# Optimization experiments

Measured on AMD Instinct MI355X. Metric: run time of the kernel, lower is better.

Reference implementation:

```python
import jax, jax.numpy as jnp
import numpy as np
from jax import lax

B, N, IN, OUT, RANK, P = 8, 7057, 1024, 1024, 64, 84
ALPHA = 1
SCALING = ALPHA / RANK
RATES = (2, 1, 4)


def _cubic(t):
    # PyTorch bicubic kernel (a = -0.75)
    a = -0.75
    at = jnp.abs(t)
    w1 = ((a + 2.0) * at - (a + 3.0)) * at * at + 1.0
    w2 = (((at - 5.0) * at + 8.0) * at - 4.0) * a
    return jnp.where(at <= 1.0, w1, jnp.where(at < 2.0, w2, 0.0))


def _resize_axis(x, out_size, axis):
    # 1-D bicubic resize along `axis`, align_corners=False, border replicate
    in_size = x.shape[axis]
    scale = in_size / out_size
    src = (jnp.arange(out_size, dtype=jnp.float32) + 0.5) * scale - 0.5
    i0 = jnp.floor(src)
    offs = jnp.arange(-1, 3, dtype=jnp.float32)[:, None]  # [4,1]
    pos = i0[None, :] + offs                              # [4,out]
    w = _cubic(src[None, :] - pos)                        # [4,out]
    idx = jnp.clip(pos.astype(jnp.int32), 0, in_size - 1)
    g = jnp.take(x, idx, axis=axis)  # axis -> (4, out)
    wshape = [1] * g.ndim
    wshape[axis] = 4
    wshape[axis + 1] = out_size
    return jnp.sum(g * w.reshape(wshape), axis=axis)


def _bicubic(x, h, w):
    # x: [B,C,H,W] -> [B,C,h,w]
    x = _resize_axis(x, h, axis=2)
    return _resize_axis(x, w, axis=3)


def _expert(x, cw, cb, rate):
    # x: [B,C,H,W]; cw: [C,C,3,3]; cb: [C]
    b, c, h, w = x.shape
    y = _bicubic(x, h * rate, w * rate)
    y = lax.conv_general_dilated(y, cw, (1, 1), [(1, 1), (1, 1)],
                                 dimension_numbers=('NCHW', 'OIHW', 'NCHW'))
    y = y + cb[None, :, None, None]
    y = _bicubic(y, h, w)
    return y.transpose(0, 2, 3, 1).reshape(b, h * w, c)  # [B,HW,C]


def setup_inputs() -> dict:
    key = jax.random.key(0)
    ks = jax.random.split(key, 9)
    return {
        'x': jax.random.normal(ks[0], (B, N, IN), dtype=jnp.float32),
        'W0': jax.random.normal(ks[1], (OUT, IN), dtype=jnp.float32) * 0.02,
        'b0': jax.random.normal(ks[2], (OUT,), dtype=jnp.float32) * 0.02,
        'W_down': jax.random.normal(ks[3], (RANK, IN), dtype=jnp.float32) * 0.02,
        'W_gate': jax.random.uniform(ks[4], (3, RANK), dtype=jnp.float32),
        'b_gate': jax.random.normal(ks[5], (3,), dtype=jnp.float32) * 0.02,
        'conv_w': jax.random.normal(ks[6], (3, RANK, RANK, 3, 3), dtype=jnp.float32) * 0.05,
        'conv_b': jax.random.normal(ks[7], (3, RANK), dtype=jnp.float32) * 0.02,
        'W_up': jax.random.normal(ks[8], (OUT, RANK), dtype=jnp.float32) * 0.02,
    }


def reference(x, W0, b0, W_down, W_gate, b_gate, conv_w, conv_b, W_up):
    out = jnp.einsum('bni,oi->bno', x, W0) + b0            # original layer
    z = jnp.einsum('bni,ri->bnr', x, W_down)               # lora_down (dropout p=0)
    cls_embed = z[:, :1]                                    # [B,1,R]
    feat = z[:, 1:].reshape(B, P, P, RANK).transpose(0, 3, 1, 2)  # [B,R,P,P]
    pooled = feat.mean(axis=(2, 3))                         # AdaptiveAvgPool2d(1)
    gate_score = pooled @ W_gate.T + b_gate                 # [B,3]
    gate_idx = jnp.argmax(gate_score, axis=-1)              # [B]
    eouts = jnp.stack([_expert(feat, conv_w[i], conv_b[i], RATES[i])
                       for i in range(3)], axis=0)          # [3,B,HW,R]
    sel = eouts[gate_idx, jnp.arange(B)] * SCALING          # [B,HW,R]
    lora = jnp.concatenate([cls_embed, sel], axis=1)        # [B,N,R]
    lora_out = jnp.einsum('bnr,or->bno', lora, W_up)
    return out + lora_out
```

## Files before the change

kernel.cpp:

```cpp
#include <hip/hip_runtime.h>
#include <stdint.h>

typedef unsigned short u16;
typedef __bf16 bf16x8 __attribute__((ext_vector_type(8)));
typedef float f32x4 __attribute__((ext_vector_type(4)));

#define B_ 8
#define N_ 7057
#define MTOT 56456
#define SCALING_F (1.0f/64.0f)

#define Z_OFF    0ull
#define LORA_OFF 14452736ull
#define GIDX_OFF 21679104ull
#define CWT_OFF  21679360ull
#define W0B_OFF  21900544ull
#define WDB_OFF  23997696ull
#define WUB_OFF  24128768ull
#define UP_OFF   24259840ull
#define CO_OFF   139865344ull
#define UPB_STRIDE ((size_t)112896 * 64)

__device__ __forceinline__ u16 f2b(float f) {
  __bf16 h = (__bf16)f;
  union { __bf16 h; u16 u; } v; v.h = h; return v.u;
}
__device__ __forceinline__ float b2f(u16 u) {
  union { uint32_t i; float f; } v; v.i = ((uint32_t)u) << 16; return v.f;
}
__device__ __forceinline__ void gload_lds16(const void* g, void* l) {
  __builtin_amdgcn_global_load_lds(
      (const __attribute__((address_space(1))) uint32_t*)g,
      (__attribute__((address_space(3))) uint32_t*)l, 16, 0, 0);
}
__device__ __forceinline__ f32x4 mfma16(bf16x8 a, bf16x8 b, f32x4 c) {
  return __builtin_amdgcn_mfma_f32_16x16x32_bf16(a, b, c, 0, 0, 0);
}
__device__ __forceinline__ void cvt_store8(u16* dst, float4 a, float4 b) {
  bf16x8 v;
  v[0] = (__bf16)a.x; v[1] = (__bf16)a.y; v[2] = (__bf16)a.z; v[3] = (__bf16)a.w;
  v[4] = (__bf16)b.x; v[5] = (__bf16)b.y; v[6] = (__bf16)b.z; v[7] = (__bf16)b.w;
  *(bf16x8*)dst = v;
}
__device__ __forceinline__ float cubicw(float t) {
  const float a = -0.75f;
  float at = fabsf(t);
  float w1 = ((a + 2.0f) * at - (a + 3.0f)) * at * at + 1.0f;
  float w2 = (((at - 5.0f) * at + 8.0f) * at - 4.0f) * a;
  return at <= 1.0f ? w1 : (at < 2.0f ? w2 : 0.0f);
}
__device__ __forceinline__ int iclamp(int v, int lo, int hi) { return v < lo ? lo : (v > hi ? hi : v); }
__device__ __forceinline__ int rate_of(int e) { return e == 0 ? 2 : (e == 1 ? 1 : 4); }

__global__ __launch_bounds__(256) void cvtall_kernel(const float* __restrict__ W0, const float* __restrict__ Wd,
                                                     const float* __restrict__ Wup, u16* __restrict__ dst) {
  int i = (blockIdx.x * 256 + threadIdx.x) * 4;
  if (i >= 1179648) return;
  const float* src;
  if (i < 1048576)      src = W0 + i;
  else if (i < 1114112) src = Wd + (i - 1048576);
  else                  src = Wup + (i - 1114112);
  float4 v = *(const float4*)src;
  union { u16 u[4]; uint2 q; } p;
  p.u[0] = f2b(v.x); p.u[1] = f2b(v.y); p.u[2] = f2b(v.z); p.u[3] = f2b(v.w);
  *(uint2*)(dst + i) = p.q;
}

__global__ __launch_bounds__(256) void zgemm_kernel(const float* __restrict__ x,
                                                    const u16* __restrict__ Wdb,
                                                    float* __restrict__ z) {
  __shared__ u16 As[64 * 32];
  __shared__ u16 Bs[64 * 32];
  const int tid = threadIdx.x;
  const int lane = tid & 63;
  const int w = tid >> 6;
  const int row0 = blockIdx.x * 64;
  f32x4 acc[4] = {{0,0,0,0},{0,0,0,0},{0,0,0,0},{0,0,0,0}};
  const int srow = tid >> 2, sk8 = tid & 3;
  int arow = row0 + srow; if (arow >= MTOT) arow = MTOT - 1;
  const float* agf = x + (size_t)arow * 1024 + sk8 * 8;
  const u16* bg = Wdb + (size_t)srow * 1024 + sk8 * 8;
  u16* al = As + tid * 8;
  u16* bl = Bs + tid * 8;
  const int klo = (lane >> 4) * 8;
  for (int k0 = 0; k0 < 1024; k0 += 32) {
    gload_lds16(bg + k0, bl);
    float4 q0 = *(const float4*)(agf + k0);
    float4 q1 = *(const float4*)(agf + k0 + 4);
    cvt_store8(al, q0, q1);
    __syncthreads();
    bf16x8 a = *(const bf16x8*)(As + (w * 16 + (lane & 15)) * 32 + klo);
#pragma unroll
    for (int fc = 0; fc < 4; ++fc) {
      bf16x8 bb = *(const bf16x8*)(Bs + (fc * 16 + (lane & 15)) * 32 + klo);
      acc[fc] = mfma16(a, bb, acc[fc]);
    }
    __syncthreads();
  }
  const int crow = (lane >> 4) * 4, ccol = lane & 15;
#pragma unroll
  for (int fc = 0; fc < 4; ++fc) {
#pragma unroll
    for (int i = 0; i < 4; ++i) {
      int gr = row0 + w * 16 + crow + i;
      if (gr < MTOT) z[(size_t)gr * 64 + fc * 16 + ccol] = acc[fc][i];
    }
  }
}

__global__ __launch_bounds__(256) void convwt_kernel(const float* __restrict__ cw, u16* __restrict__ cwt) {
  int idx = blockIdx.x * 256 + threadIdx.x;
  if (idx >= 3 * 9 * 64 * 64) return;
  int ci = idx & 63;
  int co = (idx >> 6) & 63;
  int rest = idx >> 12;
  int tap = rest % 9;
  int e = rest / 9;
  cwt[idx] = f2b(cw[((size_t)(e * 64 + co) * 64 + ci) * 9 + tap]);
}

__global__ __launch_bounds__(256) void gate1_kernel(const float* __restrict__ z, float* __restrict__ pp) {
  int b = blockIdx.y, q = blockIdx.x;
  int tid = threadIdx.x;
  int c = tid & 63, part = tid >> 6;
  const float* zb = z + (size_t)b * N_ * 64;
  int n0 = 1 + q * 126;
  float s = 0.0f;
  for (int n = n0 + part; n < n0 + 126; n += 4) s += zb[(size_t)n * 64 + c];
  __shared__ float red[4][64];
  red[part][c] = s;
  __syncthreads();
  if (tid < 64)
    pp[((size_t)b * 56 + q) * 64 + tid] = red[0][tid] + red[1][tid] + red[2][tid] + red[3][tid];
}

__global__ __launch_bounds__(64) void gate2_kernel(const float* __restrict__ pp, const float* __restrict__ z,
                                                   const float* __restrict__ Wg, const float* __restrict__ bg,
                                                   int* __restrict__ gidx, u16* __restrict__ lora) {
  int b = blockIdx.x;
  int c = threadIdx.x;
  float s = 0.0f;
  for (int q = 0; q < 56; ++q) s += pp[((size_t)b * 56 + q) * 64 + c];
  __shared__ float pl[64];
  pl[c] = s * (1.0f / 7056.0f);
  const float* zb = z + (size_t)b * N_ * 64;
  lora[(size_t)b * N_ * 64 + c] = f2b(zb[c]);
  __syncthreads();
  if (c == 0) {
    float best = 0.0f; int bi = 0;
    for (int e = 0; e < 3; ++e) {
      float sc = bg[e];
      for (int r = 0; r < 64; ++r) sc += pl[r] * Wg[e * 64 + r];
      if (e == 0 || sc > best) { best = sc; bi = e; }
    }
    gidx[b] = bi;
  }
}

__global__ __launch_bounds__(256) void up_kernel(const float* __restrict__ z, const int* __restrict__ gidx,
                                                 u16* __restrict__ up) {
  int b = blockIdx.z;
  int r = rate_of(gidx[b]);
  int H = 84 * r;
  int y = blockIdx.y; if (y >= H) return;
  int c = threadIdx.x & 63, s = threadIdx.x >> 6;
  int x0 = blockIdx.x * 16 + s * 4;
  if (x0 >= H) return;
  float inv = 1.0f / (float)r;
  float sy = (y + 0.5f) * inv - 0.5f;
  float fy = floorf(sy);
  int iy0 = (int)fy;
  float wy[4]; int yi[4];
#pragma unroll
  for (int u = 0; u < 4; ++u) { wy[u] = cubicw(sy - (fy - 1.0f + u)); yi[u] = iclamp(iy0 - 1 + u, 0, 83); }
  const float* zb = z + ((size_t)b * N_ + 1) * 64;
  u16* ub = up + (size_t)b * UPB_STRIDE;
#pragma unroll
  for (int xx = 0; xx < 4; ++xx) {
    int X = x0 + xx; if (X >= H) break;
    float sx = (X + 0.5f) * inv - 0.5f;
    float fx = floorf(sx);
    int ix0 = (int)fx;
    float acc = 0.0f;
#pragma unroll
    for (int v = 0; v < 4; ++v) {
      float wv = cubicw(sx - (fx - 1.0f + v));
      int xiv = iclamp(ix0 - 1 + v, 0, 83);
#pragma unroll
      for (int u = 0; u < 4; ++u)
        acc += wy[u] * wv * zb[((size_t)yi[u] * 84 + xiv) * 64 + c];
    }
    ub[((size_t)y * H + X) * 64 + c] = f2b(acc);
  }
}

__global__ __launch_bounds__(256) void conv_kernel(const u16* __restrict__ up, const u16* __restrict__ cwt,
                                                   const float* __restrict__ cb, const int* __restrict__ gidx,
                                                   u16* __restrict__ cvo) {
  int b = blockIdx.z;
  int e = gidx[b];
  int r = rate_of(e);
  int H = 84 * r;
  int tx = blockIdx.x, ty = blockIdx.y;
  if (tx * 8 >= H || ty * 8 >= H) return;
  __shared__ u16 halo[100 * 64];
  __shared__ u16 Bw[2][4096];
  int tid = threadIdx.x, lane = tid & 63, w = tid >> 6;
  const u16* ub = up + (size_t)b * UPB_STRIDE;
  const u16* wte = cwt + (size_t)e * 9 * 4096;
  gload_lds16(wte + tid * 8, Bw[0] + tid * 8);
  gload_lds16(wte + 2048 + tid * 8, Bw[0] + 2048 + tid * 8);
  for (int li = tid; li < 800; li += 256) {
    int pix = li >> 3, cq = li & 7;
    int hy = pix / 10, hx = pix - hy * 10;
    int iy = ty * 8 - 1 + hy, ix = tx * 8 - 1 + hx;
    uint4 v = {0u, 0u, 0u, 0u};
    if (iy >= 0 && iy < H && ix >= 0 && ix < H)
      v = *(const uint4*)(ub + ((size_t)iy * H + ix) * 64 + cq * 8);
    *(uint4*)(halo + pix * 64 + cq * 8) = v;
  }
  __syncthreads();
  f32x4 acc[4] = {{0,0,0,0},{0,0,0,0},{0,0,0,0},{0,0,0,0}};
  int p = w * 16 + (lane & 15);
  int py = p >> 3, px = p & 7;
  int klo = (lane >> 4) * 8;
  for (int tap = 0; tap < 9; ++tap) {
    if (tap < 8) {
      const u16* wt = wte + (size_t)(tap + 1) * 4096;
      gload_lds16(wt + tid * 8, Bw[(tap + 1) & 1] + tid * 8);
      gload_lds16(wt + 2048 + tid * 8, Bw[(tap + 1) & 1] + 2048 + tid * 8);
    }
    int dy = tap / 3, dx = tap - dy * 3;
    const u16* hb = halo + ((py + dy) * 10 + (px + dx)) * 64 + klo;
    const u16* bwc = Bw[tap & 1];
#pragma unroll
    for (int kk = 0; kk < 2; ++kk) {
      bf16x8 a = *(const bf16x8*)(hb + kk * 32);
#pragma unroll
      for (int fc = 0; fc < 4; ++fc) {
        bf16x8 bb = *(const bf16x8*)(bwc + (fc * 16 + (lane & 15)) * 64 + kk * 32 + klo);
        acc[fc] = mfma16(a, bb, acc[fc]);
      }
    }
    __syncthreads();
  }
  int crow = (lane >> 4) * 4, ccol = lane & 15;
  u16* cvb = cvo + (size_t)b * UPB_STRIDE;
#pragma unroll
  for (int fc = 0; fc < 4; ++fc) {
    int co = fc * 16 + ccol;
    float bias = cb[e * 64 + co];
#pragma unroll
    for (int i = 0; i < 4; ++i) {
      int pd = w * 16 + crow + i;
      int gy = ty * 8 + (pd >> 3), gx = tx * 8 + (pd & 7);
      if (gy < H && gx < H)
        cvb[((size_t)gy * H + gx) * 64 + co] = f2b(acc[fc][i] + bias);
    }
  }
}

__global__ __launch_bounds__(256) void down_kernel(const u16* __restrict__ cvo, const int* __restrict__ gidx,
                                                   u16* __restrict__ lora) {
  int b = blockIdx.z;
  int r = rate_of(gidx[b]);
  int H = 84 * r;
  int tid = threadIdx.x;
  int c = tid & 63, s = tid >> 6;
  int y = blockIdx.y;
  int x = blockIdx.x * 4 + s;
  float fr = (float)r;
  float sy = (y + 0.5f) * fr - 0.5f;
  float fy = floorf(sy);
  int iy0 = (int)fy;
  float wy[4]; int yi[4];
#pragma unroll
  for (int u = 0; u < 4; ++u) { wy[u] = cubicw(sy - (fy - 1.0f + u)); yi[u] = iclamp(iy0 - 1 + u, 0, H - 1); }
  float sx = (x + 0.5f) * fr - 0.5f;
  float fx = floorf(sx);
  int ix0 = (int)fx;
  float wx[4]; int xi[4];
#pragma unroll
  for (int v = 0; v < 4; ++v) { wx[v] = cubicw(sx - (fx - 1.0f + v)); xi[v] = iclamp(ix0 - 1 + v, 0, H - 1); }
  const u16* cbase = cvo + (size_t)b * UPB_STRIDE;
  float acc = 0.0f;
#pragma unroll
  for (int u = 0; u < 4; ++u)
#pragma unroll
    for (int v = 0; v < 4; ++v)
      acc += wy[u] * wx[v] * b2f(cbase[((size_t)yi[u] * H + xi[v]) * 64 + c]);
  lora[((size_t)b * N_ + 1 + y * 84 + x) * 64 + c] = f2b(acc * SCALING_F);
}

#define MAIN_COMPUTE()                                                                       \
  {                                                                                          \
    bf16x8 af[4], bfr[4];                                                                    \
    _Pragma("unroll")                                                                        \
    for (int fm = 0; fm < 4; ++fm)                                                           \
      af[fm] = *(const bf16x8*)(As + (wr * 64 + fm * 16 + (lane & 15)) * 32 + klo);          \
    _Pragma("unroll")                                                                        \
    for (int fc = 0; fc < 4; ++fc)                                                           \
      bfr[fc] = *(const bf16x8*)(Bs + (wc * 64 + fc * 16 + (lane & 15)) * 32 + klo);         \
    _Pragma("unroll")                                                                        \
    for (int fm = 0; fm < 4; ++fm) {                                                         \
      _Pragma("unroll")                                                                      \
      for (int fc = 0; fc < 4; ++fc)                                                         \
        acc[fm][fc] = mfma16(af[fm], bfr[fc], acc[fm][fc]);                                  \
    }                                                                                        \
  }

__global__ __launch_bounds__(256) void main_gemm(const float* __restrict__ x, const u16* __restrict__ W0b,
                                                 const float* __restrict__ b0, const u16* __restrict__ lora,
                                                 const u16* __restrict__ Wub, float* __restrict__ out) {
  __shared__ u16 As[128 * 32];
  __shared__ u16 Bs[128 * 32];
  int tid = threadIdx.x, lane = tid & 63, w = tid >> 6;
  int bid = blockIdx.x;
  int wg = (bid & 7) * 442 + (bid >> 3);
  int row0 = (wg >> 3) * 128, col0 = (wg & 7) * 128;
  int wr = w >> 1, wc = w & 1;
  f32x4 acc[4][4] = {};
  int srow = tid >> 2, sk8 = tid & 3;
  int ar0 = row0 + srow; if (ar0 >= MTOT) ar0 = MTOT - 1;
  int ar1 = row0 + srow + 64; if (ar1 >= MTOT) ar1 = MTOT - 1;
  const float* agf0 = x + (size_t)ar0 * 1024 + sk8 * 8;
  const float* agf1 = x + (size_t)ar1 * 1024 + sk8 * 8;
  const u16* bg0 = W0b + (size_t)(col0 + srow) * 1024 + sk8 * 8;
  const u16* bg1 = W0b + (size_t)(col0 + srow + 64) * 1024 + sk8 * 8;
  u16* al0 = As + tid * 8; u16* al1 = As + tid * 8 + 2048;
  u16* bl0 = Bs + tid * 8; u16* bl1 = Bs + tid * 8 + 2048;
  const int klo = (lane >> 4) * 8;
  for (int k0 = 0; k0 < 1024; k0 += 32) {
    gload_lds16(bg0 + k0, bl0);
    gload_lds16(bg1 + k0, bl1);
    float4 q0 = *(const float4*)(agf0 + k0);
    float4 q1 = *(const float4*)(agf0 + k0 + 4);
    float4 q2 = *(const float4*)(agf1 + k0);
    float4 q3 = *(const float4*)(agf1 + k0 + 4);
    cvt_store8(al0, q0, q1);
    cvt_store8(al1, q2, q3);
    __syncthreads();
    MAIN_COMPUTE();
    __syncthreads();
  }
  const u16* lg0 = lora + (size_t)ar0 * 64 + sk8 * 8;
  const u16* lg1 = lora + (size_t)ar1 * 64 + sk8 * 8;
  const u16* ug0 = Wub + (size_t)(col0 + srow) * 64 + sk8 * 8;
  const u16* ug1 = Wub + (size_t)(col0 + srow + 64) * 64 + sk8 * 8;
  for (int k0 = 0; k0 < 64; k0 += 32) {
    gload_lds16(lg0 + k0, al0);
    gload_lds16(lg1 + k0, al1);
    gload_lds16(ug0 + k0, bl0);
    gload_lds16(ug1 + k0, bl1);
    __syncthreads();
    MAIN_COMPUTE();
    __syncthreads();
  }
  int crow = (lane >> 4) * 4, ccol = lane & 15;
#pragma unroll
  for (int fm = 0; fm < 4; ++fm) {
    int grb = row0 + wr * 64 + fm * 16 + crow;
#pragma unroll
    for (int fc = 0; fc < 4; ++fc) {
      int gc = col0 + wc * 64 + fc * 16 + ccol;
      float bias = b0[gc];
#pragma unroll
      for (int i = 0; i < 4; ++i) {
        int gr = grb + i;
        if (gr < MTOT) out[(size_t)gr * 1024 + gc] = acc[fm][fc][i] + bias;
      }
    }
  }
}

extern "C" void kernel_launch(void* const* d_in, const int* in_sizes, int n_in,
                              void* d_out, int out_size, void* d_ws, size_t ws_size,
                              hipStream_t stream) {
  const float* x   = (const float*)d_in[0];
  const float* W0  = (const float*)d_in[1];
  const float* b0  = (const float*)d_in[2];
  const float* Wd  = (const float*)d_in[3];
  const float* Wg  = (const float*)d_in[4];
  const float* bg  = (const float*)d_in[5];
  const float* cw  = (const float*)d_in[6];
  const float* cb  = (const float*)d_in[7];
  const float* Wup = (const float*)d_in[8];
  char* ws = (char*)d_ws;
  float* z    = (float*)(ws + Z_OFF);
  u16* lora   = (u16*)(ws + LORA_OFF);
  int* gidx   = (int*)(ws + GIDX_OFF);
  u16* cwt    = (u16*)(ws + CWT_OFF);
  u16* W0b    = (u16*)(ws + W0B_OFF);
  u16* Wub    = (u16*)(ws + WUB_OFF);
  u16* up     = (u16*)(ws + UP_OFF);
  float* pp   = (float*)(ws + UP_OFF);
  u16* cvo    = (u16*)(ws + CO_OFF);
  float* out  = (float*)d_out;
  u16* Wdb    = (u16*)(ws + WDB_OFF);

  cvtall_kernel<<<dim3(1152), dim3(256), 0, stream>>>(W0, Wd, Wup, W0b);
  convwt_kernel<<<dim3(432), dim3(256), 0, stream>>>(cw, cwt);
  zgemm_kernel<<<dim3(883), dim3(256), 0, stream>>>(x, Wdb, z);
  gate1_kernel<<<dim3(56, 8), dim3(256), 0, stream>>>(z, pp);
  gate2_kernel<<<dim3(8), dim3(64), 0, stream>>>(pp, z, Wg, bg, gidx, lora);
  up_kernel<<<dim3(21, 336, 8), dim3(256), 0, stream>>>(z, gidx, up);
  conv_kernel<<<dim3(42, 42, 8), dim3(256), 0, stream>>>(up, cwt, cb, gidx, cvo);
  down_kernel<<<dim3(21, 84, 8), dim3(256), 0, stream>>>(cvo, gidx, lora);
  main_gemm<<<dim3(3536), dim3(256), 0, stream>>>(x, W0b, b0, lora, Wub, out);
}
```

Before: 642.9 us.

## Pre-convert x to bf16 in zgemm and stream it to main GEMM via LDS DMA

Measured after the change: 595.7 us. 1.08x faster.

```diff
diff --git a/kernel.cpp b/kernel.cpp
--- a/kernel.cpp
+++ b/kernel.cpp
@@ -19,6 +19,9 @@
 #define WUB_OFF  24128768ull
 #define UP_OFF   24259840ull
 #define CO_OFF   139865344ull
+#define XB_OFF   255470848ull
+#define WS_FAST  371092736ull
+#define WS_SLOW  255487232ull
 #define UPB_STRIDE ((size_t)112896 * 64)
 
 __device__ __forceinline__ u16 f2b(float f) {
@@ -36,11 +39,11 @@
 __device__ __forceinline__ f32x4 mfma16(bf16x8 a, bf16x8 b, f32x4 c) {
   return __builtin_amdgcn_mfma_f32_16x16x32_bf16(a, b, c, 0, 0, 0);
 }
-__device__ __forceinline__ void cvt_store8(u16* dst, float4 a, float4 b) {
+__device__ __forceinline__ bf16x8 cvt8(float4 a, float4 b) {
   bf16x8 v;
   v[0] = (__bf16)a.x; v[1] = (__bf16)a.y; v[2] = (__bf16)a.z; v[3] = (__bf16)a.w;
   v[4] = (__bf16)b.x; v[5] = (__bf16)b.y; v[6] = (__bf16)b.z; v[7] = (__bf16)b.w;
-  *(bf16x8*)dst = v;
+  return v;
 }
 __device__ __forceinline__ float cubicw(float t) {
   const float a = -0.75f;
@@ -66,9 +69,19 @@
   *(uint2*)(dst + i) = p.q;
 }
 
+__global__ __launch_bounds__(256) void cvtx_kernel(const float* __restrict__ x, u16* __restrict__ xb) {
+  size_t stride = (size_t)gridDim.x * 256 * 8;
+  for (size_t i = ((size_t)blockIdx.x * 256 + threadIdx.x) * 8; i < (size_t)MTOT * 1024; i += stride) {
+    float4 a = *(const float4*)(x + i);
+    float4 b = *(const float4*)(x + i + 4);
+    *(bf16x8*)(xb + i) = cvt8(a, b);
+  }
+}
+
 __global__ __launch_bounds__(256) void zgemm_kernel(const float* __restrict__ x,
                                                     const u16* __restrict__ Wdb,
-                                                    float* __restrict__ z) {
+                                                    float* __restrict__ z,
+                                                    u16* __restrict__ xb) {
   __shared__ u16 As[64 * 32];
   __shared__ u16 Bs[64 * 32];
   const int tid = threadIdx.x;
@@ -80,6 +93,7 @@
   int arow = row0 + srow; if (arow >= MTOT) arow = MTOT - 1;
   const float* agf = x + (size_t)arow * 1024 + sk8 * 8;
   const u16* bg = Wdb + (size_t)srow * 1024 + sk8 * 8;
+  u16* xbp = xb ? (xb + (size_t)arow * 1024 + sk8 * 8) : nullptr;
   u16* al = As + tid * 8;
   u16* bl = Bs + tid * 8;
   const int klo = (lane >> 4) * 8;
@@ -87,7 +101,9 @@
     gload_lds16(bg + k0, bl);
     float4 q0 = *(const float4*)(agf + k0);
     float4 q1 = *(const float4*)(agf + k0 + 4);
-    cvt_store8(al, q0, q1);
+    bf16x8 cv = cvt8(q0, q1);
+    *(bf16x8*)al = cv;
+    if (xbp) *(bf16x8*)(xbp + k0) = cv;
     __syncthreads();
     bf16x8 a = *(const bf16x8*)(As + (w * 16 + (lane & 15)) * 32 + klo);
 #pragma unroll
@@ -292,70 +308,80 @@
   lora[((size_t)b * N_ + 1 + y * 84 + x) * 64 + c] = f2b(acc * SCALING_F);
 }
 
-#define MAIN_COMPUTE()                                                                       \
-  {                                                                                          \
-    bf16x8 af[4], bfr[4];                                                                    \
-    _Pragma("unroll")                                                                        \
-    for (int fm = 0; fm < 4; ++fm)                                                           \
-      af[fm] = *(const bf16x8*)(As + (wr * 64 + fm * 16 + (lane & 15)) * 32 + klo);          \
-    _Pragma("unroll")                                                                        \
-    for (int fc = 0; fc < 4; ++fc)                                                           \
-      bfr[fc] = *(const bf16x8*)(Bs + (wc * 64 + fc * 16 + (lane & 15)) * 32 + klo);         \
-    _Pragma("unroll")                                                                        \
-    for (int fm = 0; fm < 4; ++fm) {                                                         \
-      _Pragma("unroll")                                                                      \
-      for (int fc = 0; fc < 4; ++fc)                                                         \
-        acc[fm][fc] = mfma16(af[fm], bfr[fc], acc[fm][fc]);                                  \
-    }                                                                                        \
-  }
-
-__global__ __launch_bounds__(256) void main_gemm(const float* __restrict__ x, const u16* __restrict__ W0b,
+__global__ __launch_bounds__(256) void main_gemm(const u16* __restrict__ xb, const u16* __restrict__ W0b,
                                                  const float* __restrict__ b0, const u16* __restrict__ lora,
                                                  const u16* __restrict__ Wub, float* __restrict__ out) {
-  __shared__ u16 As[128 * 32];
-  __shared__ u16 Bs[128 * 32];
+  __shared__ u16 As[128 * 64];
+  __shared__ u16 Bs[128 * 64];
   int tid = threadIdx.x, lane = tid & 63, w = tid >> 6;
   int bid = blockIdx.x;
   int wg = (bid & 7) * 442 + (bid >> 3);
   int row0 = (wg >> 3) * 128, col0 = (wg & 7) * 128;
   int wr = w >> 1, wc = w & 1;
   f32x4 acc[4][4] = {};
-  int srow = tid >> 2, sk8 = tid & 3;
-  int ar0 = row0 + srow; if (ar0 >= MTOT) ar0 = MTOT - 1;
-  int ar1 = row0 + srow + 64; if (ar1 >= MTOT) ar1 = MTOT - 1;
-  const float* agf0 = x + (size_t)ar0 * 1024 + sk8 * 8;
-  const float* agf1 = x + (size_t)ar1 * 1024 + sk8 * 8;
-  const u16* bg0 = W0b + (size_t)(col0 + srow) * 1024 + sk8 * 8;
-  const u16* bg1 = W0b + (size_t)(col0 + srow + 64) * 1024 + sk8 * 8;
-  u16* al0 = As + tid * 8; u16* al1 = As + tid * 8 + 2048;
-  u16* bl0 = Bs + tid * 8; u16* bl1 = Bs + tid * 8 + 2048;
-  const int klo = (lane >> 4) * 8;
-  for (int k0 = 0; k0 < 1024; k0 += 32) {
-    gload_lds16(bg0 + k0, bl0);
-    gload_lds16(bg1 + k0, bl1);
-    float4 q0 = *(const float4*)(agf0 + k0);
-    float4 q1 = *(const float4*)(agf0 + k0 + 4);
-    float4 q2 = *(const float4*)(agf1 + k0);
-    float4 q3 = *(const float4*)(agf1 + k0 + 4);
-    cvt_store8(al0, q0, q1);
-    cvt_store8(al1, q2, q3);
+  int srow = tid >> 3;
+  int schunk = tid & 7;
+  int sch8 = ((schunk ^ (srow & 7)) << 3);
+  int ar[4]; int br[4];
+  u16* aldst[4]; u16* bldst[4];
+#pragma unroll
+  for (int p = 0; p < 4; ++p) {
+    int rr = row0 + p * 32 + srow;
+    ar[p] = rr >= MTOT ? MTOT - 1 : rr;
+    br[p] = col0 + p * 32 + srow;
+    aldst[p] = As + (p * 32 + srow) * 64 + schunk * 8;
+    bldst[p] = Bs + (p * 32 + srow) * 64 + schunk * 8;
+  }
+  for (int k0 = 0; k0 < 1024; k0 += 64) {
+#pragma unroll
+    for (int p = 0; p < 4; ++p)
+      gload_lds16(xb + (size_t)ar[p] * 1024 + k0 + sch8, aldst[p]);
+#pragma unroll
+    for (int p = 0; p < 4; ++p)
+      gload_lds16(W0b + (size_t)br[p] * 1024 + k0 + sch8, bldst[p]);
     __syncthreads();
-    MAIN_COMPUTE();
+#pragma unroll
+    for (int kk = 0; kk < 2; ++kk) {
+      int pc = (((kk << 2) + (lane >> 4)) ^ (lane & 7)) << 3;
+      bf16x8 af[4], bfr[4];
+#pragma unroll
+      for (int fm = 0; fm < 4; ++fm)
+        af[fm] = *(const bf16x8*)(As + (wr * 64 + fm * 16 + (lane & 15)) * 64 + pc);
+#pragma unroll
+      for (int fc = 0; fc < 4; ++fc)
+        bfr[fc] = *(const bf16x8*)(Bs + (wc * 64 + fc * 16 + (lane & 15)) * 64 + pc);
+#pragma unroll
+      for (int fm = 0; fm < 4; ++fm)
+#pragma unroll
+        for (int fc = 0; fc < 4; ++fc)
+          acc[fm][fc] = mfma16(af[fm], bfr[fc], acc[fm][fc]);
+    }
     __syncthreads();
   }
-  const u16* lg0 = lora + (size_t)ar0 * 64 + sk8 * 8;
-  const u16* lg1 = lora + (size_t)ar1 * 64 + sk8 * 8;
-  const u16* ug0 = Wub + (size_t)(col0 + srow) * 64 + sk8 * 8;
-  const u16* ug1 = Wub + (size_t)(col0 + srow + 64) * 64 + sk8 * 8;
-  for (int k0 = 0; k0 < 64; k0 += 32) {
-    gload_lds16(lg0 + k0, al0);
-    gload_lds16(lg1 + k0, al1);
-    gload_lds16(ug0 + k0, bl0);
-    gload_lds16(ug1 + k0, bl1);
-    __syncthreads();
-    MAIN_COMPUTE();
-    __syncthreads();
-  }
+#pragma unroll
+  for (int p = 0; p < 4; ++p)
+    gload_lds16(lora + (size_t)ar[p] * 64 + sch8, aldst[p]);
+#pragma unroll
+  for (int p = 0; p < 4; ++p)
+    gload_lds16(Wub + (size_t)br[p] * 64 + sch8, bldst[p]);
+  __syncthreads();
+#pragma unroll
+  for (int kk = 0; kk < 2; ++kk) {
+    int pc = (((kk << 2) + (lane >> 4)) ^ (lane & 7)) << 3;
+    bf16x8 af[4], bfr[4];
+#pragma unroll
+    for (int fm = 0; fm < 4; ++fm)
+      af[fm] = *(const bf16x8*)(As + (wr * 64 + fm * 16 + (lane & 15)) * 64 + pc);
+#pragma unroll
+    for (int fc = 0; fc < 4; ++fc)
+      bfr[fc] = *(const bf16x8*)(Bs + (wc * 64 + fc * 16 + (lane & 15)) * 64 + pc);
+#pragma unroll
+    for (int fm = 0; fm < 4; ++fm)
+#pragma unroll
+      for (int fc = 0; fc < 4; ++fc)
+        acc[fm][fc] = mfma16(af[fm], bfr[fc], acc[fm][fc]);
+  }
+  __syncthreads();
   int crow = (lane >> 4) * 4, ccol = lane & 15;
 #pragma unroll
   for (int fm = 0; fm < 4; ++fm) {
@@ -391,20 +417,25 @@
   int* gidx   = (int*)(ws + GIDX_OFF);
   u16* cwt    = (u16*)(ws + CWT_OFF);
   u16* W0b    = (u16*)(ws + W0B_OFF);
+  u16* Wdb    = (u16*)(ws + WDB_OFF);
   u16* Wub    = (u16*)(ws + WUB_OFF);
   u16* up     = (u16*)(ws + UP_OFF);
   float* pp   = (float*)(ws + UP_OFF);
   u16* cvo    = (u16*)(ws + CO_OFF);
   float* out  = (float*)d_out;
-  u16* Wdb    = (u16*)(ws + WDB_OFF);
+
+  const bool fast = ws_size >= WS_FAST;
+  u16* xb = fast ? (u16*)(ws + XB_OFF) : (u16*)(ws + CO_OFF);
 
   cvtall_kernel<<<dim3(1152), dim3(256), 0, stream>>>(W0, Wd, Wup, W0b);
   convwt_kernel<<<dim3(432), dim3(256), 0, stream>>>(cw, cwt);
-  zgemm_kernel<<<dim3(883), dim3(256), 0, stream>>>(x, Wdb, z);
+  zgemm_kernel<<<dim3(883), dim3(256), 0, stream>>>(x, Wdb, z, fast ? xb : nullptr);
   gate1_kernel<<<dim3(56, 8), dim3(256), 0, stream>>>(z, pp);
   gate2_kernel<<<dim3(8), dim3(64), 0, stream>>>(pp, z, Wg, bg, gidx, lora);
   up_kernel<<<dim3(21, 336, 8), dim3(256), 0, stream>>>(z, gidx, up);
   conv_kernel<<<dim3(42, 42, 8), dim3(256), 0, stream>>>(up, cwt, cb, gidx, cvo);
   down_kernel<<<dim3(21, 84, 8), dim3(256), 0, stream>>>(cvo, gidx, lora);
-  main_gemm<<<dim3(3536), dim3(256), 0, stream>>>(x, W0b, b0, lora, Wub, out);
-}
+  if (!fast)
+    cvtx_kernel<<<dim3(2048), dim3(256), 0, stream>>>(x, xb);
+  main_gemm<<<dim3(3536), dim3(256), 0, stream>>>(xb, W0b, b0, lora, Wub, out);
+}
```
